# Performance work log

Hardware: AMD Instinct MI355X
Metric: run time of the kernel (lower is better)

## Reference

```python
import math
import jax, jax.numpy as jnp
import numpy as np

IN_DIM = 512
OUT_DIM = 512
K = 3
EPS = 1e-8


def setup_inputs() -> dict:
    key = jax.random.key(0)
    k1, k2, k3 = jax.random.split(key, 3)
    b, h, w = 8, 64, 64
    x = jax.random.normal(k1, (b, IN_DIM, h, w), dtype=jnp.float32)
    style = jax.random.normal(k2, (b, IN_DIM), dtype=jnp.float32)
    weight = jax.random.normal(k3, (OUT_DIM, IN_DIM, K, K), dtype=jnp.float32)
    bias = jnp.zeros((OUT_DIM,), dtype=jnp.float32)
    return {"x": x, "style": style, "weight": weight, "bias": bias}


def _mod_weights(weight, style):
    # EqualizedWeight scaling: c = 1/sqrt(prod(shape[1:]))
    c = 1.0 / math.sqrt(IN_DIM * K * K)
    w = weight * c                                    # [out, in, k, k]
    ws = w[None] * (style[:, None, :, None, None] + 1.0)  # [b, out, in, k, k]
    sigma_inv = jax.lax.rsqrt(jnp.sum(ws * ws, axis=(2, 3, 4), keepdims=True) + EPS)
    return ws * sigma_inv


def reference(x, style, weight, bias):
    ws = _mod_weights(weight, style)                  # [b, out, in, k, k]

    def conv_one(xi, wi):
        # xi: [in, h, w], wi: [out, in, k, k]
        y = jax.lax.conv_general_dilated(
            xi[None], wi, window_strides=(1, 1), padding="SAME",
            dimension_numbers=("NCHW", "OIHW", "NCHW"))
        return y[0]

    out = jax.vmap(conv_one)(x, ws)                   # [b, out, h, w]
    return out + bias[None, :, None, None]
```

## Files before the change

kernel.cpp:

```cpp
#include <hip/hip_runtime.h>

#define CIN 512
#define COUT 512
#define HH 64
#define WW 64
#define BB 8
#define KTOT 4608

#define XPD 66
#define BUFSH (10 * 66 * 32)
#define BUFB  (BUFSH * 2)
#define ROWB  (66 * 64)

typedef __attribute__((ext_vector_type(8))) short short8;
typedef __attribute__((ext_vector_type(4))) float f32x4;

__device__ inline unsigned short f2bf(float f) {
    unsigned int u = __float_as_uint(f);
    u += 0x7FFFu + ((u >> 16) & 1u);
    return (unsigned short)(u >> 16);
}

__device__ inline void gll16(const void* g, void* l) {
    __builtin_amdgcn_global_load_lds(
        (const __attribute__((address_space(1))) unsigned int*)g,
        (__attribute__((address_space(3))) unsigned int*)l, 16, 0, 0);
}

__global__ __launch_bounds__(256) void zring_kernel(unsigned short* __restrict__ xtp) {
    const int e = blockIdx.x * 256 + threadIdx.x;
    if (e >= BB * 260 * 64) return;
    const int unit = e & 63;
    const int sa = e >> 6;
    const int b = sa / 260;
    const int s = sa - b * 260;
    int yy, xx;
    if (s < 66)       { yy = 0;        xx = s; }
    else if (s < 132) { yy = 65;       xx = s - 66; }
    else if (s < 196) { yy = s - 131;  xx = 0; }
    else              { yy = s - 195;  xx = 65; }
    *(short8*)(xtp + ((size_t)(b * XPD + yy) * XPD + xx) * 512 + unit * 8) =
        (short8){0, 0, 0, 0, 0, 0, 0, 0};
}

__global__ __launch_bounds__(256) void xpose_kernel(const float* __restrict__ x,
                                                    const float* __restrict__ style,
                                                    unsigned short* __restrict__ xtp) {
    __shared__ float tile[32 * 65];
    __shared__ float sst[32];
    const int ic = blockIdx.x;
    const int y  = blockIdx.y;
    const int b  = blockIdx.z;
    const int t  = threadIdx.x;
    if (t < 32) sst[t] = style[b * CIN + ic * 32 + t] + 1.0f;
#pragma unroll
    for (int it = 0; it < 8; ++it) {
        int e = it * 256 + t;
        int ii = e >> 6, xx = e & 63;
        tile[ii * 65 + xx] = x[(((size_t)(b * CIN + ic * 32 + ii) * HH + y) << 6) + xx];
    }
    __syncthreads();
#pragma unroll
    for (int it = 0; it < 8; ++it) {
        int g = it * 256 + t;
        int xx = g >> 5, ii = g & 31;
        xtp[((size_t)(b * XPD + y + 1) * XPD + xx + 1) * 512 + ic * 32 + ii] =
            f2bf(tile[ii * 65 + xx] * sst[ii]);
    }
}

__global__ __launch_bounds__(256) void wpack_kernel(const float* __restrict__ weight,
                                                    unsigned short* __restrict__ wpk) {
    __shared__ float q[KTOT];
    const int o = blockIdx.x;
    const int t = threadIdx.x;
    const float* wrow = weight + (size_t)o * KTOT;
    const float cst = 1.0f / sqrtf((float)KTOT);
#pragma unroll
    for (int it = 0; it < 18; ++it) {
        int e = it * 256 + t;
        q[e] = wrow[e] * cst;
    }
    __syncthreads();
    const int g = o >> 4, l15 = o & 15;
    for (int m = t; m < 576; m += 256) {
        int c   = m / 36;
        int rem = m - c * 36;
        int tap = rem >> 2;
        int l4  = rem & 3;
        short8 v;
#pragma unroll
        for (int e = 0; e < 8; ++e)
            v[e] = (short)f2bf(q[(c * 32 + l4 * 8 + e) * 9 + tap]);
        *(short8*)(wpk + ((((size_t)c * 9 + tap) * 32 + g) * 64 + l4 * 16 + l15) * 8) = v;
    }
}

__global__ __launch_bounds__(256) void sigma_kernel(const float* __restrict__ weight,
                                                    const float* __restrict__ style,
                                                    float* __restrict__ siginv) {
    __shared__ float sred[4][8];
    const int o = blockIdx.x;
    const int t = threadIdx.x;
    const float* wrow = weight + (size_t)o * KTOT;
    float acc[8] = {0.f, 0.f, 0.f, 0.f, 0.f, 0.f, 0.f, 0.f};
#pragma unroll
    for (int ii = 0; ii < 2; ++ii) {
        const int i = t * 2 + ii;
        float wsq = 0.f;
#pragma unroll
        for (int tap = 0; tap < 9; ++tap) {
            float v = wrow[i * 9 + tap];
            wsq += v * v;
        }
#pragma unroll
        for (int b = 0; b < 8; ++b) {
            float s = style[b * CIN + i] + 1.0f;
            acc[b] += wsq * s * s;
        }
    }
#pragma unroll
    for (int b = 0; b < 8; ++b) {
        float v = acc[b];
#pragma unroll
        for (int off = 32; off > 0; off >>= 1) v += __shfl_down(v, off, 64);
        if ((t & 63) == 0) sred[t >> 6][b] = v;
    }
    __syncthreads();
    if (t < 8) {
        const float S = sred[0][t] + sred[1][t] + sred[2][t] + sred[3][t];
        siginv[t * COUT + o] = rsqrtf(S * (1.0f / (float)KTOT) + 1e-8f);
    }
}

__global__ __launch_bounds__(512, 2) void conv_kernel(const unsigned short* __restrict__ wpk,
                                                      const unsigned short* __restrict__ xtp,
                                                      const float* __restrict__ siginv,
                                                      const float* __restrict__ bias,
                                                      float* __restrict__ out) {
    __shared__ __align__(16) unsigned short xs[2 * BUFSH];
    const int bid = blockIdx.x;
    const int k  = bid & 7;
    const int t  = bid >> 3;
    const int ob = k & 3;
    const int b  = (k >> 2) * 4 + (t >> 3);
    const int rg = t & 7;
    const int y0r = rg * 8;

    const int tid  = threadIdx.x;
    const int lane = tid & 63;
    const int wid_u = __builtin_amdgcn_readfirstlane(tid >> 6);
    const int l15 = lane & 15, l4 = lane >> 4;
    const int og = wid_u & 1, rp = wid_u >> 1;
    const int g0 = ob * 8 + og * 4;

    const int u = lane & 3;
    const unsigned short* srcq[5];
#pragma unroll
    for (int t4 = 0; t4 < 5; ++t4) {
        const int sl = (wid_u + t4 * 8) * 16 + (lane >> 2);
        const int row = sl / 66, col = sl - row * 66;
        srcq[t4] = xtp + ((size_t)(b * XPD + y0r + row) * XPD + col) * 512 +
                   (u ^ ((col >> 1) & 3)) * 8;
    }
    const unsigned short* srcX = xtp;
    if (wid_u <= 1) {
        const int sl = (40 + wid_u) * 16 + (lane >> 2);
        const int row = sl / 66, col = sl - row * 66;
        const int rowc = (row < 10) ? row : 9;
        srcX = xtp + ((size_t)(b * XPD + y0r + rowc) * XPD + col) * 512 +
               (u ^ ((col >> 1) & 3)) * 8;
    }

    const char* vBp[3];
#pragma unroll
    for (int kx = 0; kx < 3; ++kx)
        vBp[kx] = (const char*)xs + rp * (2 * ROWB) + (l15 + kx) * 64 +
                  ((l4 ^ (((l15 + kx) >> 1) & 3)) * 16);

    f32x4 acc[4][8];
#pragma unroll
    for (int mi = 0; mi < 4; ++mi)
#pragma unroll
        for (int j = 0; j < 8; ++j) acc[mi][j] = (f32x4){0.f, 0.f, 0.f, 0.f};

    short8 af[3][4];

    const unsigned short* aP = wpk + (size_t)g0 * 512 + lane * 8;

#define STAGE(bufp, icq)                                                                  \
    do {                                                                                  \
        unsigned short* db = xs + (bufp) * BUFSH;                                         \
        _Pragma("unroll") for (int t4 = 0; t4 < 5; ++t4)                                  \
            gll16(srcq[t4] + (size_t)(icq) * 32, db + (wid_u + t4 * 8) * 512);            \
        if (wid_u == 0)                                                                   \
            gll16(srcX + (size_t)(icq) * 32, db + 40 * 512);                              \
        else if (wid_u == 1 && lane < 16)                                                 \
            gll16(srcX + (size_t)(icq) * 32, db + 41 * 512);                              \
    } while (0)

#define TAPPHASE(tp, P, aIC)                                                              \
    do {                                                                                  \
        const unsigned short* pA = (aIC) + (size_t)((tp) + 2) * 16384;                    \
        _Pragma("unroll") for (int mi = 0; mi < 4; ++mi)                                  \
            af[((tp) + 2) % 3][mi] = *(const short8*)(pA + mi * 512);                     \
        short8 bfr[8];                                                                    \
        _Pragma("unroll") for (int j = 0; j < 8; ++j)                                     \
            bfr[j] = *(const short8*)(vBp[(tp) % 3] + (P) * BUFB +                        \
                ((tp) / 3 + (j >> 2)) * ROWB + (j & 3) * 1024);                           \
        __builtin_amdgcn_s_setprio(1);                                                    \
        _Pragma("unroll") for (int mi = 0; mi < 4; ++mi)                                  \
            _Pragma("unroll") for (int j = 0; j < 8; ++j)                                 \
                acc[mi][j] = __builtin_amdgcn_mfma_f32_16x16x32_bf16(                     \
                    af[(tp) % 3][mi], bfr[j], acc[mi][j], 0, 0, 0);                       \
        __builtin_amdgcn_s_setprio(0);                                                    \
    } while (0)

#define ICBODY(icv, P)                                                                    \
    do {                                                                                  \
        if ((icv) < 15) STAGE((P) ^ 1, (icv) + 1);                                        \
        const unsigned short* aIC = aP + (size_t)(icv) * (9 * 16384);                     \
        TAPPHASE(0, P, aIC); TAPPHASE(1, P, aIC); TAPPHASE(2, P, aIC);                    \
        TAPPHASE(3, P, aIC); TAPPHASE(4, P, aIC); TAPPHASE(5, P, aIC);                    \
        TAPPHASE(6, P, aIC); TAPPHASE(7, P, aIC); TAPPHASE(8, P, aIC);                    \
        __syncthreads();                                                                  \
    } while (0)

#pragma unroll
    for (int mi = 0; mi < 4; ++mi) af[0][mi] = *(const short8*)(aP + mi * 512);
#pragma unroll
    for (int mi = 0; mi < 4; ++mi) af[1][mi] = *(const short8*)(aP + 16384 + mi * 512);
    STAGE(0, 0);
    __syncthreads();

#pragma unroll 1
    for (int ic = 0; ic < 16; ic += 2) {
        ICBODY(ic, 0);
        ICBODY(ic + 1, 1);
    }

    const int yb0 = y0r + rp * 2;
#pragma unroll
    for (int mi = 0; mi < 4; ++mi) {
        const int obase = ob * 128 + og * 64 + mi * 16 + l4 * 4;
#pragma unroll
        for (int rr = 0; rr < 4; ++rr) {
            const int o = obase + rr;
            const float sv = siginv[b * COUT + o];
            const float bv = bias[o];
#pragma unroll
            for (int j = 0; j < 8; ++j) {
                const int yout = yb0 + (j >> 2);
                out[(((size_t)(b * COUT + o) * HH + yout) << 6) + (j & 3) * 16 + l15] =
                    acc[mi][j][rr] * sv + bv;
            }
        }
    }
#undef STAGE
#undef TAPPHASE
#undef ICBODY
}

extern "C" void kernel_launch(void* const* d_in, const int* in_sizes, int n_in,
                              void* d_out, int out_size, void* d_ws, size_t ws_size,
                              hipStream_t stream) {
    const float* x      = (const float*)d_in[0];
    const float* style  = (const float*)d_in[1];
    const float* weight = (const float*)d_in[2];
    const float* bias   = (const float*)d_in[3];
    float* out = (float*)d_out;

    unsigned short* wpk = (unsigned short*)d_ws;
    unsigned short* xtp = wpk + (size_t)2359296;
    float* siginv = (float*)(xtp + (size_t)BB * XPD * XPD * 512);

    zring_kernel<<<520, 256, 0, stream>>>(xtp);
    xpose_kernel<<<dim3(16, HH, BB), 256, 0, stream>>>(x, style, xtp);
    wpack_kernel<<<COUT, 256, 0, stream>>>(weight, wpk);
    sigma_kernel<<<COUT, 256, 0, stream>>>(weight, style, siginv);
    conv_kernel<<<256, 512, 0, stream>>>(wpk, xtp, siginv, bias, out);
}
```

Before: 167.0 us.

## Shrink conv tiles to two output rows per block with 256 threads

Each conv block now computes 2 output rows instead of 8, using 4 waves instead of 8 and half the accumulators per wave. The grid grows from 256 to 1024 blocks, and the LDS halo buffer shrinks to 4 padded rows. The aim is more blocks per CU and better occupancy and load balance through smaller LDS and register footprints. The cost is more halo re-reads (4 rows loaded per 2 computed) and more weight reloads per output, which raises global and L2 traffic.

```diff
diff --git a/kernel.cpp b/kernel.cpp
--- a/kernel.cpp
+++ b/kernel.cpp
@@ -8,7 +8,7 @@
 #define KTOT 4608
 
 #define XPD 66
-#define BUFSH (10 * 66 * 32)
+#define BUFSH (4 * 66 * 32)
 #define BUFB  (BUFSH * 2)
 #define ROWB  (66 * 64)
 
@@ -133,7 +133,7 @@
     }
 }
 
-__global__ __launch_bounds__(512, 2) void conv_kernel(const unsigned short* __restrict__ wpk,
+__global__ __launch_bounds__(256, 3) void conv_kernel(const unsigned short* __restrict__ wpk,
                                                       const unsigned short* __restrict__ xtp,
                                                       const float* __restrict__ siginv,
                                                       const float* __restrict__ bias,
@@ -143,9 +143,8 @@
     const int k  = bid & 7;
     const int t  = bid >> 3;
     const int ob = k & 3;
-    const int b  = (k >> 2) * 4 + (t >> 3);
-    const int rg = t & 7;
-    const int y0r = rg * 8;
+    const int b  = (k >> 2) * 4 + (t >> 5);
+    const int y0 = (t & 31) * 2;
 
     const int tid  = threadIdx.x;
     const int lane = tid & 63;
@@ -154,35 +153,31 @@
     const int og = wid_u & 1, rp = wid_u >> 1;
     const int g0 = ob * 8 + og * 4;
 
-    const int u = lane & 3;
-    const unsigned short* srcq[5];
-#pragma unroll
-    for (int t4 = 0; t4 < 5; ++t4) {
-        const int sl = (wid_u + t4 * 8) * 16 + (lane >> 2);
+    const unsigned short* srcq[4];
+#pragma unroll
+    for (int q = 0; q < 4; ++q) {
+        const int L = q * 256 + wid_u * 64 + lane;
+        const int sl = L >> 2, u = L & 3;
         const int row = sl / 66, col = sl - row * 66;
-        srcq[t4] = xtp + ((size_t)(b * XPD + y0r + row) * XPD + col) * 512 +
-                   (u ^ ((col >> 1) & 3)) * 8;
-    }
-    const unsigned short* srcX = xtp;
-    if (wid_u <= 1) {
-        const int sl = (40 + wid_u) * 16 + (lane >> 2);
-        const int row = sl / 66, col = sl - row * 66;
-        const int rowc = (row < 10) ? row : 9;
-        srcX = xtp + ((size_t)(b * XPD + y0r + rowc) * XPD + col) * 512 +
-               (u ^ ((col >> 1) & 3)) * 8;
-    }
+        srcq[q] = xtp + ((size_t)(b * XPD + y0 + row) * XPD + col) * 512 +
+                  (u ^ ((col >> 1) & 3)) * 8;
+    }
+    const int colR = 58 + (lane >> 2);
+    const unsigned short* srcR =
+        xtp + ((size_t)(b * XPD + y0 + 3) * XPD + colR) * 512 +
+        ((lane & 3) ^ ((colR >> 1) & 3)) * 8;
 
     const char* vBp[3];
 #pragma unroll
     for (int kx = 0; kx < 3; ++kx)
-        vBp[kx] = (const char*)xs + rp * (2 * ROWB) + (l15 + kx) * 64 +
+        vBp[kx] = (const char*)xs + rp * ROWB + (l15 + kx) * 64 +
                   ((l4 ^ (((l15 + kx) >> 1) & 3)) * 16);
 
-    f32x4 acc[4][8];
+    f32x4 acc[4][4];
 #pragma unroll
     for (int mi = 0; mi < 4; ++mi)
 #pragma unroll
-        for (int j = 0; j < 8; ++j) acc[mi][j] = (f32x4){0.f, 0.f, 0.f, 0.f};
+        for (int j = 0; j < 4; ++j) acc[mi][j] = (f32x4){0.f, 0.f, 0.f, 0.f};
 
     short8 af[3][4];
 
@@ -191,12 +186,10 @@
 #define STAGE(bufp, icq)                                                                  \
     do {                                                                                  \
         unsigned short* db = xs + (bufp) * BUFSH;                                         \
-        _Pragma("unroll") for (int t4 = 0; t4 < 5; ++t4)                                  \
-            gll16(srcq[t4] + (size_t)(icq) * 32, db + (wid_u + t4 * 8) * 512);            \
-        if (wid_u == 0)                                                                   \
-            gll16(srcX + (size_t)(icq) * 32, db + 40 * 512);                              \
-        else if (wid_u == 1 && lane < 16)                                                 \
-            gll16(srcX + (size_t)(icq) * 32, db + 41 * 512);                              \
+        _Pragma("unroll") for (int q = 0; q < 4; ++q)                                     \
+            gll16(srcq[q] + (size_t)(icq) * 32, db + q * 2048 + wid_u * 512);             \
+        if (wid_u == 0 && lane < 32)                                                      \
+            gll16(srcR + (size_t)(icq) * 32, db + 8192);                                  \
     } while (0)
 
 #define TAPPHASE(tp, P, aIC)                                                              \
@@ -204,13 +197,13 @@
         const unsigned short* pA = (aIC) + (size_t)((tp) + 2) * 16384;                    \
         _Pragma("unroll") for (int mi = 0; mi < 4; ++mi)                                  \
             af[((tp) + 2) % 3][mi] = *(const short8*)(pA + mi * 512);                     \
-        short8 bfr[8];                                                                    \
-        _Pragma("unroll") for (int j = 0; j < 8; ++j)                                     \
-            bfr[j] = *(const short8*)(vBp[(tp) % 3] + (P) * BUFB +                        \
-                ((tp) / 3 + (j >> 2)) * ROWB + (j & 3) * 1024);                           \
+        short8 bfr[4];                                                                    \
+        const char* bp = vBp[(tp) % 3] + (P) * BUFB + ((tp) / 3) * ROWB;                  \
+        _Pragma("unroll") for (int j = 0; j < 4; ++j)                                     \
+            bfr[j] = *(const short8*)(bp + j * 1024);                                     \
         __builtin_amdgcn_s_setprio(1);                                                    \
         _Pragma("unroll") for (int mi = 0; mi < 4; ++mi)                                  \
-            _Pragma("unroll") for (int j = 0; j < 8; ++j)                                 \
+            _Pragma("unroll") for (int j = 0; j < 4; ++j)                                 \
                 acc[mi][j] = __builtin_amdgcn_mfma_f32_16x16x32_bf16(                     \
                     af[(tp) % 3][mi], bfr[j], acc[mi][j], 0, 0, 0);                       \
         __builtin_amdgcn_s_setprio(0);                                                    \
@@ -234,12 +227,12 @@
     __syncthreads();
 
 #pragma unroll 1
-    for (int ic = 0; ic < 16; ic += 2) {
-        ICBODY(ic, 0);
-        ICBODY(ic + 1, 1);
-    }
-
-    const int yb0 = y0r + rp * 2;
+    for (int icp = 0; icp < 8; ++icp) {
+        ICBODY(icp * 2, 0);
+        ICBODY(icp * 2 + 1, 1);
+    }
+
+    const int yout = y0 + rp;
 #pragma unroll
     for (int mi = 0; mi < 4; ++mi) {
         const int obase = ob * 128 + og * 64 + mi * 16 + l4 * 4;
@@ -248,11 +241,10 @@
             const int o = obase + rr;
             const float sv = siginv[b * COUT + o];
             const float bv = bias[o];
-#pragma unroll
-            for (int j = 0; j < 8; ++j) {
-                const int yout = yb0 + (j >> 2);
-                out[(((size_t)(b * COUT + o) * HH + yout) << 6) + (j & 3) * 16 + l15] =
-                    acc[mi][j][rr] * sv + bv;
+            float* orow = out + (((size_t)(b * COUT + o) * HH + yout) << 6);
+#pragma unroll
+            for (int j = 0; j < 4; ++j) {
+                orow[j * 16 + l15] = acc[mi][j][rr] * sv + bv;
             }
         }
     }
@@ -278,5 +270,5 @@
     xpose_kernel<<<dim3(16, HH, BB), 256, 0, stream>>>(x, style, xtp);
     wpack_kernel<<<COUT, 256, 0, stream>>>(weight, wpk);
     sigma_kernel<<<COUT, 256, 0, stream>>>(weight, style, siginv);
-    conv_kernel<<<256, 512, 0, stream>>>(wpk, xtp, siginv, bias, out);
-}
+    conv_kernel<<<1024, 256, 0, stream>>>(wpk, xtp, siginv, bias, out);
+}
```

Measured after the change: 189.4 us. 1.13x slower.
